# Optimization experiments

Hardware: AMD Instinct MI355X
Metric: run time of the kernel (lower is better)

The kernel has to match this reference:

```python
import jax, jax.numpy as jnp
import numpy as np

B, C, H, W = 4, 64, 128, 128
D_INNER, D_STATE, DT_RANK, K = 192, 16, 6, 4  # d_model = 3*C//2 = 96, expand = 2
EPS = 1e-5


def _haar():
    # pywt db1: dec_lo=[s,s], dec_hi=[-s,s]; code reverses dec_* and uses rec_* in
    # original order -> for Haar both dec and rec filter banks are identical.
    s = np.float32(1.0 / np.sqrt(2.0))
    lo = np.array([s, s], np.float32)
    hi = np.array([s, -s], np.float32)
    # stack order: [lo(i)lo(j), hi(i)lo(j), lo(i)hi(j), hi(i)hi(j)]
    return np.stack([np.outer(lo, lo), np.outer(hi, lo),
                     np.outer(lo, hi), np.outer(hi, hi)], 0)  # (4,2,2)

DEC = jnp.asarray(_haar())
REC = jnp.asarray(_haar())
DN = ('NCHW', 'OIHW', 'NCHW')


def _ln(x, s, b):
    m = x.mean(-1, keepdims=True)
    v = x.var(-1, keepdims=True)
    return (x - m) * jax.lax.rsqrt(v + EPS) * s + b


def _wt(x):
    b, c, h, w = x.shape
    wf = jnp.tile(DEC[:, None], (c, 1, 1, 1))  # (4c,1,2,2), groups=c, pad=0 for db1
    y = jax.lax.conv_general_dilated(x, wf, (2, 2), 'VALID',
                                     feature_group_count=c, dimension_numbers=DN)
    return y.reshape(b, c, 4, h // 2, w // 2)


def _iwt(x):
    # conv_transpose2d(stride=2, pad=0, groups=c) == lhs-dilated conv with flipped kernel, pad k-1
    b, c = x.shape[0], x.shape[1]
    h2, w2 = x.shape[3], x.shape[4]
    xr = x.reshape(b, c * 4, h2, w2)
    wf = jnp.tile(REC[:, ::-1, ::-1][None], (c, 1, 1, 1))  # (c,4,2,2)
    return jax.lax.conv_general_dilated(xr, wf, (1, 1), ((1, 1), (1, 1)),
                                        lhs_dilation=(2, 2), feature_group_count=c,
                                        dimension_numbers=DN)


def _ss2d(x, in_proj_w, conv_dw_w, conv_dw_b, x_proj_w, dt_proj_w, dt_proj_b,
          A_log, Ds, out_norm_s, out_norm_b, out_proj_w):
    b, d, h, w = x.shape  # d == D_INNER
    L = h * w
    xz = jnp.einsum('bchw,ec->behw', x, in_proj_w)  # (b,2d,h,w)
    x1, z = xz[:, :d], xz[:, d:]
    x1 = jax.lax.conv_general_dilated(x1, conv_dw_w, (1, 1), ((1, 1), (1, 1)),
                                      feature_group_count=d, dimension_numbers=DN)
    x1 = jax.nn.silu(x1 + conv_dw_b[None, :, None, None])
    # 4-direction flattening: hw, wh, and their reverses
    xf = x1.reshape(b, d, L)
    xt = x1.transpose(0, 1, 3, 2).reshape(b, d, L)
    xs = jnp.stack([xf, xt], 1)
    xs = jnp.concatenate([xs, xs[..., ::-1]], 1)  # (b,K,d,L)
    x_dbl = jnp.einsum('bkdl,kcd->bkcl', xs, x_proj_w)
    dts = x_dbl[:, :, :DT_RANK]
    Bs = x_dbl[:, :, DT_RANK:DT_RANK + D_STATE]   # (b,K,n,L)
    Cs = x_dbl[:, :, DT_RANK + D_STATE:]
    delta = jax.nn.softplus(jnp.einsum('bkrl,kdr->bkdl', dts, dt_proj_w)
                            + dt_proj_b[None, :, :, None])
    A = -jnp.exp(A_log)  # (K,d,n)

    def step(hc, inp):
        d_t, u_t, b_t, c_t = inp  # (b,K,d),(b,K,d),(b,K,n),(b,K,n)
        dA = jnp.exp(d_t[..., None] * A[None])
        hc = hc * dA + (d_t * u_t)[..., None] * b_t[:, :, None, :]
        y = jnp.einsum('bkdn,bkn->bkd', hc, c_t)
        return hc, y

    h0 = jnp.zeros((b, K, d, D_STATE), x.dtype)
    inputs = (delta.transpose(3, 0, 1, 2), xs.transpose(3, 0, 1, 2),
              Bs.transpose(3, 0, 1, 2), Cs.transpose(3, 0, 1, 2))
    _, ys = jax.lax.scan(step, h0, inputs)            # (L,b,K,d)
    out_y = ys.transpose(1, 2, 3, 0) + xs * Ds[None, :, :, None]  # (b,K,d,L)
    inv_y = out_y[:, 2:][..., ::-1]
    wh = out_y[:, 1].reshape(b, d, w, h).transpose(0, 1, 3, 2).reshape(b, d, L)
    invwh = inv_y[:, 1].reshape(b, d, w, h).transpose(0, 1, 3, 2).reshape(b, d, L)
    y = out_y[:, 0] + inv_y[:, 0] + wh + invwh        # (b,d,L)
    y = _ln(y.reshape(b, d, h, w).transpose(0, 2, 3, 1), out_norm_s, out_norm_b)
    y = y * jax.nn.silu(z.transpose(0, 2, 3, 1))
    y = jnp.einsum('bhwd,ed->bhwe', y, out_proj_w)
    return y.transpose(0, 3, 1, 2)


def reference(x, wt_low_scale, wt_high_scale, low_conv_w, in_proj_w, conv_dw_w,
              conv_dw_b, x_proj_w, dt_proj_w, dt_proj_b, A_log, Ds,
              out_norm_s, out_norm_b, out_proj_w, ln2_s, ln2_b, eca_w):
    b, c = x.shape[0], x.shape[1]
    wt = _wt(x)                                       # (b,c,4,h2,w2)
    h2, w2 = wt.shape[3], wt.shape[4]
    low = wt[:, :, 0] * wt_low_scale
    high = wt[:, :, 1:].reshape(b, c * 3, h2, w2) * wt_high_scale
    low = jax.nn.silu(jnp.einsum('bchw,ec->behw', low, low_conv_w[:, :, 0, 0]))
    high = _ss2d(high, in_proj_w, conv_dw_w, conv_dw_b, x_proj_w, dt_proj_w,
                 dt_proj_b, A_log, Ds, out_norm_s, out_norm_b, out_proj_w)
    high = _ln(high.transpose(0, 2, 3, 1), ln2_s, ln2_b).transpose(0, 3, 1, 2)
    mamba = jnp.tile(low, (1, 3, 1, 1)) * high
    merged = jnp.concatenate([low, mamba], 1).reshape(b, c, 4, h2, w2)
    y = _iwt(merged)                                  # (b,c,h,w)
    # ECA: gap -> conv1d(k=5) over channels -> sigmoid gate
    pooled = y.mean((2, 3))[:, None, :]               # (b,1,c)
    att = jax.lax.conv_general_dilated(pooled, eca_w.reshape(1, 1, 5), (1,),
                                       ((2, 2),), dimension_numbers=('NCH', 'OIH', 'NCH'))
    att = jax.nn.sigmoid(att[:, 0])
    return y * att[:, :, None, None] + x


def setup_inputs():
    key = jax.random.key(0)
    ks = jax.random.split(key, 20)
    f = jax.random.normal
    return {
        'x': f(ks[0], (B, C, H, W), jnp.float32),
        'wt_low_scale': jax.random.uniform(ks[1], (1, C, 1, 1), jnp.float32),
        'wt_high_scale': jax.random.uniform(ks[2], (1, 3 * C, 1, 1), jnp.float32),
        'low_conv_w': f(ks[3], (C, C, 1, 1), jnp.float32) * 0.1,
        'in_proj_w': f(ks[4], (2 * D_INNER, D_INNER), jnp.float32) * 0.05,
        'conv_dw_w': f(ks[5], (D_INNER, 1, 3, 3), jnp.float32) * 0.3,
        'conv_dw_b': f(ks[6], (D_INNER,), jnp.float32) * 0.1,
        'x_proj_w': f(ks[7], (K, DT_RANK + 2 * D_STATE, D_INNER), jnp.float32) * 0.05,
        'dt_proj_w': f(ks[8], (K, D_INNER, DT_RANK), jnp.float32) * 0.1,
        'dt_proj_b': jax.random.uniform(ks[9], (K, D_INNER), jnp.float32) - 4.0,
        'A_log': jax.random.uniform(ks[10], (K, D_INNER, D_STATE), jnp.float32),
        'Ds': f(ks[11], (K, D_INNER), jnp.float32) * 0.1,
        'out_norm_s': jnp.ones((D_INNER,), jnp.float32),
        'out_norm_b': jnp.zeros((D_INNER,), jnp.float32),
        'out_proj_w': f(ks[12], (D_INNER, D_INNER), jnp.float32) * 0.05,
        'ln2_s': jnp.ones((3 * C,), jnp.float32),
        'ln2_b': jnp.zeros((3 * C,), jnp.float32),
        'eca_w': f(ks[13], (5,), jnp.float32) * 0.3,
    }
```

## Files before the change

kernel.cpp:

```cpp
#include <hip/hip_runtime.h>

constexpr int cB = 4, cC = 64, cH = 128, cW = 128;
constexpr int cL = 4096;
constexpr int cD = 192, cN = 16;
constexpr int NCH = 64, CHUNK = 64;

__device__ __forceinline__ float silu_f(float v) { return v / (1.f + __expf(-v)); }

__global__ __launch_bounds__(256) void k_wt(const float* __restrict__ x,
                                            const float* __restrict__ wls,
                                            const float* __restrict__ whs,
                                            float* __restrict__ lraw,
                                            float* __restrict__ high) {
    int idx = blockIdx.x * 256 + threadIdx.x;
    int j = idx & 63, i = (idx >> 6) & 63, c = (idx >> 12) & 63, b = idx >> 18;
    const float* xp = x + (((size_t)(b * cC + c)) * cH + 2 * i) * cW + 2 * j;
    float x00 = xp[0], x01 = xp[1], x10 = xp[cW], x11 = xp[cW + 1];
    float s0 = 0.5f * (x00 + x01 + x10 + x11);
    float s1 = 0.5f * (x00 + x01 - x10 - x11);
    float s2 = 0.5f * (x00 - x01 + x10 - x11);
    float s3 = 0.5f * (x00 - x01 - x10 + x11);
    int l = i * 64 + j;
    lraw[(size_t)(b * cC + c) * cL + l] = s0 * wls[c];
    int ch = c * 3;
    high[(size_t)(b * cD + ch + 0) * cL + l] = s1 * whs[ch + 0];
    high[(size_t)(b * cD + ch + 1) * cL + l] = s2 * whs[ch + 1];
    high[(size_t)(b * cD + ch + 2) * cL + l] = s3 * whs[ch + 2];
}

__global__ __launch_bounds__(256) void k_lowconv(const float* __restrict__ lraw,
                                                 const float* __restrict__ w,
                                                 float* __restrict__ lowT) {
    int bid = blockIdx.x;
    int lt0 = (bid & 63) * 64;
    int b = bid >> 6;
    __shared__ float sW[16][68];
    __shared__ float sI[16][65];
    int tid = threadIdx.x, lt = tid & 63, eg = tid >> 6;
    float acc[16];
#pragma unroll
    for (int m = 0; m < 16; m++) acc[m] = 0.f;
    for (int c0 = 0; c0 < 64; c0 += 16) {
#pragma unroll
        for (int q = 0; q < 4; q++) {
            int tt = tid + q * 256;
            int cc = tt & 15, ee = tt >> 4;
            sW[cc][ee] = w[ee * 64 + c0 + cc];
        }
#pragma unroll
        for (int q = 0; q < 4; q++) {
            int tt = tid + q * 256;
            int ll = tt & 63, cc = tt >> 6;
            sI[cc][ll] = lraw[(size_t)(b * cC + c0 + cc) * cL + lt0 + ll];
        }
        __syncthreads();
#pragma unroll
        for (int cc = 0; cc < 16; cc++) {
            float iv = sI[cc][lt];
#pragma unroll
            for (int m = 0; m < 16; m++) acc[m] = fmaf(sW[cc][eg * 16 + m], iv, acc[m]);
        }
        __syncthreads();
    }
#pragma unroll
    for (int m = 0; m < 16; m++) {
        int e = eg * 16 + m;
        lowT[((size_t)b * cL + lt0 + lt) * 64 + e] = silu_f(acc[m]);
    }
}

__global__ __launch_bounds__(256) void k_inproj(const float* __restrict__ hi,
                                                const float* __restrict__ w,
                                                float* __restrict__ xout,
                                                float* __restrict__ zT) {
    int bid = blockIdx.x;
    int lt0 = (bid & 63) * 64;
    int et = (bid >> 6) % 6;
    int b = bid / (6 * 64);
    int e0 = et * 64;
    __shared__ float sW[16][68];
    __shared__ float sI[16][65];
    int tid = threadIdx.x, lt = tid & 63, eg = tid >> 6;
    float acc[16];
#pragma unroll
    for (int m = 0; m < 16; m++) acc[m] = 0.f;
    for (int c0 = 0; c0 < 192; c0 += 16) {
#pragma unroll
        for (int q = 0; q < 4; q++) {
            int tt = tid + q * 256;
            int cc = tt & 15, ee = tt >> 4;
            sW[cc][ee] = w[(e0 + ee) * 192 + c0 + cc];
        }
#pragma unroll
        for (int q = 0; q < 4; q++) {
            int tt = tid + q * 256;
            int ll = tt & 63, cc = tt >> 6;
            sI[cc][ll] = hi[(size_t)(b * cD + c0 + cc) * cL + lt0 + ll];
        }
        __syncthreads();
#pragma unroll
        for (int cc = 0; cc < 16; cc++) {
            float iv = sI[cc][lt];
#pragma unroll
            for (int m = 0; m < 16; m++) acc[m] = fmaf(sW[cc][eg * 16 + m], iv, acc[m]);
        }
        __syncthreads();
    }
#pragma unroll
    for (int m = 0; m < 16; m++) {
        int e = e0 + eg * 16 + m;
        float v = acc[m];
        if (e < 192) xout[(size_t)(b * cD + e) * cL + lt0 + lt] = v;
        else zT[((size_t)b * cL + lt0 + lt) * 192 + (e - 192)] = v;
    }
}

__global__ __launch_bounds__(256) void k_dwconv(const float* __restrict__ xin,
                                                const float* __restrict__ w,
                                                const float* __restrict__ bias,
                                                float* __restrict__ x1,
                                                float* __restrict__ u1) {
    int bd = blockIdx.x;
    int d = bd % cD;
    const float* xp = xin + (size_t)bd * cL;
    float wv[9];
#pragma unroll
    for (int t = 0; t < 9; t++) wv[t] = w[d * 9 + t];
    float bv = bias[d];
    __shared__ float sm[64][65];
    int tid = threadIdx.x;
#pragma unroll
    for (int q = 0; q < 16; q++) {
        int p = tid + q * 256;
        int i = p >> 6, j = p & 63;
        float acc = bv;
#pragma unroll
        for (int di = 0; di < 3; di++) {
            int ii = i + di - 1;
            if (ii < 0 || ii >= 64) continue;
#pragma unroll
            for (int dj = 0; dj < 3; dj++) {
                int jj = j + dj - 1;
                if (jj < 0 || jj >= 64) continue;
                acc = fmaf(wv[di * 3 + dj], xp[ii * 64 + jj], acc);
            }
        }
        sm[i][j] = silu_f(acc);
    }
    __syncthreads();
#pragma unroll
    for (int q = 0; q < 16; q++) {
        int p = tid + q * 256;
        x1[(size_t)bd * cL + p] = sm[p >> 6][p & 63];
        u1[(size_t)bd * cL + p] = sm[p & 63][p >> 6];
    }
}

__global__ __launch_bounds__(256) void k_xproj(const float* __restrict__ x1,
                                               const float* __restrict__ u1,
                                               const float* __restrict__ xpw,
                                               float* __restrict__ xdbl) {
    int bid = blockIdx.x;
    int lt0 = (bid & 63) * 64;
    int k = (bid >> 6) & 3;
    int b = bid >> 8;
    const float* src = (k & 1) ? u1 : x1;
    bool rev = (k >= 2);
    __shared__ float sW[16][68];
    __shared__ float sI[16][65];
    int tid = threadIdx.x, lt = tid & 63, eg = tid >> 6;
    float acc[16];
#pragma unroll
    for (int m = 0; m < 16; m++) acc[m] = 0.f;
    for (int c0 = 0; c0 < 192; c0 += 16) {
#pragma unroll
        for (int q = 0; q < 4; q++) {
            int tt = tid + q * 256;
            int cc = tt & 15, ee = tt >> 4;
            sW[cc][ee] = (ee < 38) ? xpw[(k * 38 + ee) * 192 + c0 + cc] : 0.f;
        }
#pragma unroll
        for (int q = 0; q < 4; q++) {
            int tt = tid + q * 256;
            int ll = tt & 63, cc = tt >> 6;
            int l = lt0 + ll;
            int lm = rev ? (cL - 1 - l) : l;
            sI[cc][ll] = src[(size_t)(b * cD + c0 + cc) * cL + lm];
        }
        __syncthreads();
#pragma unroll
        for (int cc = 0; cc < 16; cc++) {
            float iv = sI[cc][lt];
#pragma unroll
            for (int m = 0; m < 16; m++) acc[m] = fmaf(sW[cc][eg * 16 + m], iv, acc[m]);
        }
        __syncthreads();
    }
#pragma unroll
    for (int m = 0; m < 16; m++) {
        int e = eg * 16 + m;
        if (e < 38) xdbl[(size_t)((b * 4 + k) * 38 + e) * cL + lt0 + lt] = acc[m];
    }
}

__global__ __launch_bounds__(384) void k_scan1(const float* __restrict__ xdbl,
                                               const float* __restrict__ x1,
                                               const float* __restrict__ u1,
                                               const float* __restrict__ dtw,
                                               const float* __restrict__ dtb,
                                               const float* __restrict__ alog,
                                               float* __restrict__ P,
                                               float* __restrict__ S) {
    int bid = blockIdx.x;
    int ch = bid % NCH;
    int bk = bid / NCH;
    int k = bk & 3, b = bk >> 2;
    int tid = threadIdx.x;
    int d = tid % 192, nh = tid / 192;
    int n0 = nh * 8;
    float Av2[8], h[8], Pe[8];
#pragma unroll
    for (int j = 0; j < 8; j++) {
        Av2[j] = -__expf(alog[(k * 192 + d) * 16 + n0 + j]) * 1.44269504088896f;
        h[j] = 0.f;
        Pe[j] = 0.f;
    }
    float dtbv = dtb[k * 192 + d];
    float dtwv[6];
#pragma unroll
    for (int r = 0; r < 6; r++) dtwv[r] = dtw[(k * 192 + d) * 6 + r];
    const float* dtrows = xdbl + (size_t)(bk * 38) * cL;
    const float* Brow = xdbl + (size_t)(bk * 38 + 6) * cL;
    const float* usrc = ((k & 1) ? u1 : x1) + (size_t)b * cD * cL;
    bool rev = (k >= 2);

    __shared__ float su[192][17];
    __shared__ float sB[16][16];
    __shared__ float sdt[16][8];

    int p0 = ch * CHUNK;
    for (int t0 = p0; t0 < p0 + CHUNK; t0 += 16) {
#pragma unroll
        for (int pp = 0; pp < 8; pp++) {
            int row = pp * 24 + (tid >> 4);
            int col = tid & 15;
            su[row][col] = usrc[(size_t)row * cL + (rev ? (cL - 1 - (t0 + col)) : (t0 + col))];
        }
        if (tid < 256) sB[tid & 15][tid >> 4] = Brow[(size_t)(tid >> 4) * cL + t0 + (tid & 15)];
        if (tid < 96) sdt[tid & 15][tid >> 4] = dtrows[(size_t)(tid >> 4) * cL + t0 + (tid & 15)];
        __syncthreads();
#pragma unroll
        for (int l = 0; l < 16; l++) {
            float uv = su[d][l];
            float acc = dtbv;
#pragma unroll
            for (int r = 0; r < 6; r++) acc = fmaf(dtwv[r], sdt[l][r], acc);
            float sp = fmaxf(acc, 0.f) + __logf(1.f + __expf(-fabsf(acc)));
            float duB = sp * uv;
            float Bv[8];
            *reinterpret_cast<float4*>(&Bv[0]) = *reinterpret_cast<const float4*>(&sB[l][n0]);
            *reinterpret_cast<float4*>(&Bv[4]) = *reinterpret_cast<const float4*>(&sB[l][n0 + 4]);
#pragma unroll
            for (int j = 0; j < 8; j++) {
                float e = sp * Av2[j];
                Pe[j] += e;
                float dA = exp2f(e);
                h[j] = fmaf(h[j], dA, duB * Bv[j]);
            }
        }
        __syncthreads();
    }
    size_t base = (size_t)bid * 16 * 192 + d;
#pragma unroll
    for (int j = 0; j < 8; j++) {
        P[base + (size_t)(n0 + j) * 192] = exp2f(Pe[j]);
        S[base + (size_t)(n0 + j) * 192] = h[j];
    }
}

__global__ __launch_bounds__(256) void k_carry(const float* __restrict__ P,
                                               float* __restrict__ S) {
    int gid = blockIdx.x * 256 + threadIdx.x;
    int d = gid % 192;
    int n = (gid / 192) & 15;
    int bk = gid / 3072;
    float h = 0.f;
    for (int c = 0; c < NCH; c++) {
        size_t idx = ((size_t)(bk * NCH + c) * 16 + n) * 192 + d;
        h = fmaf(P[idx], h, S[idx]);
        S[idx] = h;
    }
}

__global__ __launch_bounds__(384) void k_scan2(const float* __restrict__ xdbl,
                                               const float* __restrict__ x1,
                                               const float* __restrict__ u1,
                                               const float* __restrict__ dtw,
                                               const float* __restrict__ dtb,
                                               const float* __restrict__ alog,
                                               const float* __restrict__ dss,
                                               const float* __restrict__ S,
                                               float* __restrict__ yacc) {
    int bid = blockIdx.x;
    int ch = bid % NCH;
    int bk = bid / NCH;
    int k = bk & 3, b = bk >> 2;
    int tid = threadIdx.x;
    int d = tid % 192, nh = tid / 192;
    int n0 = nh * 8;
    float Av2[8], h[8];
#pragma unroll
    for (int j = 0; j < 8; j++) {
        Av2[j] = -__expf(alog[(k * 192 + d) * 16 + n0 + j]) * 1.44269504088896f;
        h[j] = (ch == 0) ? 0.f : S[((size_t)(bk * NCH + ch - 1) * 16 + n0 + j) * 192 + d];
    }
    float Dv = dss[k * 192 + d];
    float dtbv = dtb[k * 192 + d];
    float dtwv[6];
#pragma unroll
    for (int r = 0; r < 6; r++) dtwv[r] = dtw[(k * 192 + d) * 6 + r];
    const float* dtrows = xdbl + (size_t)(bk * 38) * cL;
    const float* Brow = xdbl + (size_t)(bk * 38 + 6) * cL;
    const float* Crow = xdbl + (size_t)(bk * 38 + 22) * cL;
    const float* usrc = ((k & 1) ? u1 : x1) + (size_t)b * cD * cL;
    bool rev = (k >= 2);

    __shared__ float su[192][17];
    __shared__ float sB[16][16];
    __shared__ float sC[16][16];
    __shared__ float sdt[16][8];

    int p0 = ch * CHUNK;
    for (int t0 = p0; t0 < p0 + CHUNK; t0 += 16) {
#pragma unroll
        for (int pp = 0; pp < 8; pp++) {
            int row = pp * 24 + (tid >> 4);
            int col = tid & 15;
            su[row][col] = usrc[(size_t)row * cL + (rev ? (cL - 1 - (t0 + col)) : (t0 + col))];
        }
        if (tid < 256) {
            sB[tid & 15][tid >> 4] = Brow[(size_t)(tid >> 4) * cL + t0 + (tid & 15)];
            sC[tid & 15][tid >> 4] = Crow[(size_t)(tid >> 4) * cL + t0 + (tid & 15)];
        }
        if (tid < 96) sdt[tid & 15][tid >> 4] = dtrows[(size_t)(tid >> 4) * cL + t0 + (tid & 15)];
        __syncthreads();
#pragma unroll
        for (int l = 0; l < 16; l++) {
            float uv = su[d][l];
            float acc = dtbv;
#pragma unroll
            for (int r = 0; r < 6; r++) acc = fmaf(dtwv[r], sdt[l][r], acc);
            float sp = fmaxf(acc, 0.f) + __logf(1.f + __expf(-fabsf(acc)));
            float duB = sp * uv;
            float Bv[8], Cv[8];
            *reinterpret_cast<float4*>(&Bv[0]) = *reinterpret_cast<const float4*>(&sB[l][n0]);
            *reinterpret_cast<float4*>(&Bv[4]) = *reinterpret_cast<const float4*>(&sB[l][n0 + 4]);
            *reinterpret_cast<float4*>(&Cv[0]) = *reinterpret_cast<const float4*>(&sC[l][n0]);
            *reinterpret_cast<float4*>(&Cv[4]) = *reinterpret_cast<const float4*>(&sC[l][n0 + 4]);
            float y = (nh == 0) ? uv * Dv : 0.f;
#pragma unroll
            for (int j = 0; j < 8; j++) {
                float dA = exp2f(sp * Av2[j]);
                h[j] = fmaf(h[j], dA, duB * Bv[j]);
                y = fmaf(h[j], Cv[j], y);
            }
            int lg = t0 + l;
            int lm;
            if (k == 0) lm = lg;
            else if (k == 1) lm = (lg & 63) * 64 + (lg >> 6);
            else if (k == 2) lm = cL - 1 - lg;
            else { int q = cL - 1 - lg; lm = (q & 63) * 64 + (q >> 6); }
            atomicAdd(&yacc[((size_t)b * cL + lm) * 192 + d], y);
        }
        __syncthreads();
    }
}

__global__ __launch_bounds__(256) void k_comb(const float* __restrict__ yacc,
                                              const float* __restrict__ zT,
                                              const float* __restrict__ ons,
                                              const float* __restrict__ onb,
                                              float* __restrict__ yln) {
    int bid = blockIdx.x;
    int b = bid >> 10;
    int pg = bid & 1023;
    int tid = threadIdx.x;
    int wq = tid >> 6, lane = tid & 63;
    int l = pg * 4 + wq;
    float v[3];
    float s = 0.f, s2 = 0.f;
#pragma unroll
    for (int m = 0; m < 3; m++) {
        int d = lane + 64 * m;
        float t = yacc[((size_t)b * cL + l) * 192 + d];
        v[m] = t;
        s += t;
        s2 += t * t;
    }
#pragma unroll
    for (int o = 1; o < 64; o <<= 1) {
        s += __shfl_xor(s, o);
        s2 += __shfl_xor(s2, o);
    }
    float mean = s / 192.f;
    float var = s2 / 192.f - mean * mean;
    float rstd = rsqrtf(var + 1e-5f);
#pragma unroll
    for (int m = 0; m < 3; m++) {
        int d = lane + 64 * m;
        float zv = zT[((size_t)b * cL + l) * 192 + d];
        float yn = (v[m] - mean) * rstd * ons[d] + onb[d];
        yln[((size_t)b * cL + l) * 192 + d] = yn * silu_f(zv);
    }
}

__global__ __launch_bounds__(256) void k_outproj(const float* __restrict__ yln,
                                                 const float* __restrict__ w,
                                                 float* __restrict__ hout) {
    int bid = blockIdx.x;
    int lt0 = (bid & 63) * 64;
    int et = (bid >> 6) % 3;
    int b = bid / 192;
    int e0 = et * 64;
    __shared__ float sW[16][68];
    __shared__ float sI[16][65];
    int tid = threadIdx.x, lt = tid & 63, eg = tid >> 6;
    float acc[16];
#pragma unroll
    for (int m = 0; m < 16; m++) acc[m] = 0.f;
    for (int c0 = 0; c0 < 192; c0 += 16) {
#pragma unroll
        for (int q = 0; q < 4; q++) {
            int tt = tid + q * 256;
            int cc = tt & 15, ee = tt >> 4;
            sW[cc][ee] = w[(e0 + ee) * 192 + c0 + cc];
        }
#pragma unroll
        for (int q = 0; q < 4; q++) {
            int tt = tid + q * 256;
            int cc = tt & 15, lq = tt >> 4;
            sI[cc][lq] = yln[((size_t)b * cL + lt0 + lq) * 192 + c0 + cc];
        }
        __syncthreads();
#pragma unroll
        for (int cc = 0; cc < 16; cc++) {
            float iv = sI[cc][lt];
#pragma unroll
            for (int m = 0; m < 16; m++) acc[m] = fmaf(sW[cc][eg * 16 + m], iv, acc[m]);
        }
        __syncthreads();
    }
#pragma unroll
    for (int m = 0; m < 16; m++) {
        hout[((size_t)b * cL + lt0 + lt) * 192 + e0 + eg * 16 + m] = acc[m];
    }
}

__global__ __launch_bounds__(256) void k_ln2(const float* __restrict__ hout,
                                             const float* __restrict__ lowT,
                                             const float* __restrict__ l2s,
                                             const float* __restrict__ l2b,
                                             float* __restrict__ merged) {
    int bid = blockIdx.x;
    int b = bid >> 10;
    int pg = bid & 1023;
    int tid = threadIdx.x;
    int wq = tid >> 6, lane = tid & 63;
    int l = pg * 4 + wq;
    float v[3];
    float s = 0.f, s2 = 0.f;
#pragma unroll
    for (int m = 0; m < 3; m++) {
        int d = lane + 64 * m;
        float t = hout[((size_t)b * cL + l) * 192 + d];
        v[m] = t;
        s += t;
        s2 += t * t;
    }
#pragma unroll
    for (int o = 1; o < 64; o <<= 1) {
        s += __shfl_xor(s, o);
        s2 += __shfl_xor(s2, o);
    }
    float mean = s / 192.f;
    float var = s2 / 192.f - mean * mean;
    float rstd = rsqrtf(var + 1e-5f);
    float lv = lowT[((size_t)b * cL + l) * 64 + lane];
    float* mp = merged + ((size_t)b * cL + l) * 256;
    mp[lane] = lv;
#pragma unroll
    for (int m = 0; m < 3; m++) {
        int d = lane + 64 * m;
        float hn = (v[m] - mean) * rstd * l2s[d] + l2b[d];
        mp[64 + d] = lv * hn;
    }
}

__global__ __launch_bounds__(256) void k_iwt(const float* __restrict__ merged,
                                             float* __restrict__ ypre) {
    int idx = blockIdx.x * 256 + threadIdx.x;
    int j = idx & 63, i = (idx >> 6) & 63, g = (idx >> 12) & 63, b = idx >> 18;
    const float4 mv = *reinterpret_cast<const float4*>(merged + ((size_t)b * cL + i * 64 + j) * 256 + g * 4);
    float m0 = mv.x, m1 = mv.y, m2 = mv.z, m3 = mv.w;
    float* yp = ypre + ((size_t)(b * 64 + g) * cH + 2 * i) * cW + 2 * j;
    float2 r0 = make_float2(0.5f * (m0 + m1 + m2 + m3), 0.5f * (m0 + m1 - m2 - m3));
    float2 r1 = make_float2(0.5f * (m0 - m1 + m2 - m3), 0.5f * (m0 - m1 - m2 + m3));
    *reinterpret_cast<float2*>(yp) = r0;
    *reinterpret_cast<float2*>(yp + cW) = r1;
}

__global__ __launch_bounds__(256) void k_pool(const float* __restrict__ ypre,
                                              float* __restrict__ pooled) {
    int bg = blockIdx.x;
    const float* p = ypre + (size_t)bg * (cH * cW);
    float s = 0.f;
    for (int t = threadIdx.x; t < cH * cW; t += 256) s += p[t];
#pragma unroll
    for (int o = 1; o < 64; o <<= 1) s += __shfl_xor(s, o);
    __shared__ float red[4];
    if ((threadIdx.x & 63) == 0) red[threadIdx.x >> 6] = s;
    __syncthreads();
    if (threadIdx.x == 0) pooled[bg] = (red[0] + red[1] + red[2] + red[3]) * (1.f / (cH * cW));
}

__global__ __launch_bounds__(256) void k_eca(const float* __restrict__ pooled,
                                             const float* __restrict__ w,
                                             float* __restrict__ att) {
    int t = threadIdx.x;
    int b = t >> 6, c = t & 63;
    float s = 0.f;
#pragma unroll
    for (int u = 0; u < 5; u++) {
        int cc = c + u - 2;
        if (cc >= 0 && cc < 64) s += w[u] * pooled[b * 64 + cc];
    }
    att[t] = 1.f / (1.f + __expf(-s));
}

__global__ __launch_bounds__(256) void k_final(const float* __restrict__ ypre,
                                               const float* __restrict__ x,
                                               const float* __restrict__ att,
                                               float* __restrict__ out) {
    int idx = blockIdx.x * 256 + threadIdx.x;
    size_t base = (size_t)idx * 4;
    int bc = (int)(base >> 14);
    float a = att[bc];
    float4 yv = *reinterpret_cast<const float4*>(ypre + base);
    float4 xv = *reinterpret_cast<const float4*>(x + base);
    float4 o;
    o.x = fmaf(yv.x, a, xv.x);
    o.y = fmaf(yv.y, a, xv.y);
    o.z = fmaf(yv.z, a, xv.z);
    o.w = fmaf(yv.w, a, xv.w);
    *reinterpret_cast<float4*>(out + base) = o;
}

extern "C" void kernel_launch(void* const* d_in, const int* in_sizes, int n_in,
                              void* d_out, int out_size, void* d_ws, size_t ws_size,
                              hipStream_t stream) {
    const float* x    = (const float*)d_in[0];
    const float* wls  = (const float*)d_in[1];
    const float* whs  = (const float*)d_in[2];
    const float* lcw  = (const float*)d_in[3];
    const float* ipw  = (const float*)d_in[4];
    const float* dww  = (const float*)d_in[5];
    const float* dwb  = (const float*)d_in[6];
    const float* xpw  = (const float*)d_in[7];
    const float* dtw  = (const float*)d_in[8];
    const float* dtb  = (const float*)d_in[9];
    const float* alog = (const float*)d_in[10];
    const float* dss  = (const float*)d_in[11];
    const float* ons  = (const float*)d_in[12];
    const float* onb  = (const float*)d_in[13];
    const float* opw  = (const float*)d_in[14];
    const float* l2s  = (const float*)d_in[15];
    const float* l2b  = (const float*)d_in[16];
    const float* ecw  = (const float*)d_in[17];
    float* out = (float*)d_out;
    float* w = (float*)d_ws;

    float* high   = w + 0;
    float* lraw   = w + 3145728;
    float* lowT   = w + 4194304;
    float* xbuf   = w + 5242880;
    float* zT     = w + 8388608;
    float* x1     = w + 11534336;
    float* u1     = w + 14680064;
    float* yacc   = w + 17825792;
    float* Sbuf   = w + 20971520;
    float* xdbl   = high;
    float* Pbuf   = xbuf;
    float* yln    = xbuf;
    float* hout   = high;
    float* merged = x1;
    float* ypre   = yacc;
    float* pooled = lraw;
    float* att    = lraw + 256;

    k_wt<<<4096, 256, 0, stream>>>(x, wls, whs, lraw, high);
    k_lowconv<<<256, 256, 0, stream>>>(lraw, lcw, lowT);
    k_inproj<<<1536, 256, 0, stream>>>(high, ipw, xbuf, zT);
    k_dwconv<<<768, 256, 0, stream>>>(xbuf, dww, dwb, x1, u1);
    k_xproj<<<1024, 256, 0, stream>>>(x1, u1, xpw, xdbl);
    hipMemsetAsync(yacc, 0, (size_t)cB * cL * cD * sizeof(float), stream);
    k_scan1<<<1024, 384, 0, stream>>>(xdbl, x1, u1, dtw, dtb, alog, Pbuf, Sbuf);
    k_carry<<<192, 256, 0, stream>>>(Pbuf, Sbuf);
    k_scan2<<<1024, 384, 0, stream>>>(xdbl, x1, u1, dtw, dtb, alog, dss, Sbuf, yacc);
    k_comb<<<4096, 256, 0, stream>>>(yacc, zT, ons, onb, yln);
    k_outproj<<<768, 256, 0, stream>>>(yln, opw, hout);
    k_ln2<<<4096, 256, 0, stream>>>(hout, lowT, l2s, l2b, merged);
    k_iwt<<<4096, 256, 0, stream>>>(merged, ypre);
    k_pool<<<256, 256, 0, stream>>>(ypre, pooled);
    k_eca<<<1, 256, 0, stream>>>(pooled, ecw, att);
    k_final<<<4096, 256, 0, stream>>>(ypre, x, att, out);
}
```

Baseline: 455.3 us.

## Double-buffer scan chunk loads through registers and batch softplus in scan kernels

Both chunked selective-scan kernels now prefetch the next 16-step tile of u, B, C and dt into registers while the current tile is processed from a double-buffered shared-memory copy. This removes the second barrier per tile and hides global-load latency behind the recurrence. The softplus of dt is computed for eight steps at once to expose more independent work before the serial state update. The in-projection kernel also reorders its block index so the six output-channel tiles of one position tile run adjacently, which may improve input reuse in cache. The cost is twice the shared memory and more registers, which may lower occupancy.

Result: no change. 452.6 us (-0.6%).

```diff
diff --git a/kernel.cpp b/kernel.cpp
--- a/kernel.cpp
+++ b/kernel.cpp
@@ -74,9 +74,10 @@
                                                 float* __restrict__ xout,
                                                 float* __restrict__ zT) {
     int bid = blockIdx.x;
-    int lt0 = (bid & 63) * 64;
-    int et = (bid >> 6) % 6;
-    int b = bid / (6 * 64);
+    int et = bid % 6;
+    int blt = bid / 6;
+    int lt0 = (blt & 63) * 64;
+    int b = blt >> 6;
     int e0 = et * 64;
     __shared__ float sW[16][68];
     __shared__ float sI[16][65];
@@ -234,41 +235,69 @@
     const float* usrc = ((k & 1) ? u1 : x1) + (size_t)b * cD * cL;
     bool rev = (k >= 2);
 
-    __shared__ float su[192][17];
-    __shared__ float sB[16][16];
-    __shared__ float sdt[16][8];
-
+    __shared__ float su[2][192][17];
+    __shared__ float sB[2][16][16];
+    __shared__ float sdt[2][16][8];
+
+    int rowA = tid >> 4, colA = tid & 15;
     int p0 = ch * CHUNK;
+    float r_su[8], r_b, r_dt;
+
+    {
+        int t0 = p0;
+#pragma unroll
+        for (int pp = 0; pp < 8; pp++) {
+            int row = pp * 24 + rowA;
+            r_su[pp] = usrc[(size_t)row * cL + (rev ? (cL - 1 - (t0 + colA)) : (t0 + colA))];
+        }
+        if (tid < 256) r_b = Brow[(size_t)rowA * cL + t0 + colA];
+        if (tid < 96)  r_dt = dtrows[(size_t)rowA * cL + t0 + colA];
+    }
+    int cur = 0;
     for (int t0 = p0; t0 < p0 + CHUNK; t0 += 16) {
 #pragma unroll
-        for (int pp = 0; pp < 8; pp++) {
-            int row = pp * 24 + (tid >> 4);
-            int col = tid & 15;
-            su[row][col] = usrc[(size_t)row * cL + (rev ? (cL - 1 - (t0 + col)) : (t0 + col))];
-        }
-        if (tid < 256) sB[tid & 15][tid >> 4] = Brow[(size_t)(tid >> 4) * cL + t0 + (tid & 15)];
-        if (tid < 96) sdt[tid & 15][tid >> 4] = dtrows[(size_t)(tid >> 4) * cL + t0 + (tid & 15)];
-        __syncthreads();
-#pragma unroll
-        for (int l = 0; l < 16; l++) {
-            float uv = su[d][l];
-            float acc = dtbv;
-#pragma unroll
-            for (int r = 0; r < 6; r++) acc = fmaf(dtwv[r], sdt[l][r], acc);
-            float sp = fmaxf(acc, 0.f) + __logf(1.f + __expf(-fabsf(acc)));
-            float duB = sp * uv;
-            float Bv[8];
-            *reinterpret_cast<float4*>(&Bv[0]) = *reinterpret_cast<const float4*>(&sB[l][n0]);
-            *reinterpret_cast<float4*>(&Bv[4]) = *reinterpret_cast<const float4*>(&sB[l][n0 + 4]);
-#pragma unroll
-            for (int j = 0; j < 8; j++) {
-                float e = sp * Av2[j];
-                Pe[j] += e;
-                float dA = exp2f(e);
-                h[j] = fmaf(h[j], dA, duB * Bv[j]);
-            }
-        }
-        __syncthreads();
+        for (int pp = 0; pp < 8; pp++) su[cur][pp * 24 + rowA][colA] = r_su[pp];
+        if (tid < 256) sB[cur][colA][rowA] = r_b;
+        if (tid < 96)  sdt[cur][colA][rowA] = r_dt;
+        __syncthreads();
+        if (t0 + 16 < p0 + CHUNK) {
+            int t1 = t0 + 16;
+#pragma unroll
+            for (int pp = 0; pp < 8; pp++) {
+                int row = pp * 24 + rowA;
+                r_su[pp] = usrc[(size_t)row * cL + (rev ? (cL - 1 - (t1 + colA)) : (t1 + colA))];
+            }
+            if (tid < 256) r_b = Brow[(size_t)rowA * cL + t1 + colA];
+            if (tid < 96)  r_dt = dtrows[(size_t)rowA * cL + t1 + colA];
+        }
+#pragma unroll
+        for (int hh = 0; hh < 2; hh++) {
+            float sp[8];
+#pragma unroll
+            for (int q = 0; q < 8; q++) {
+                int l = hh * 8 + q;
+                float acc = dtbv;
+#pragma unroll
+                for (int r = 0; r < 6; r++) acc = fmaf(dtwv[r], sdt[cur][l][r], acc);
+                sp[q] = fmaxf(acc, 0.f) + __logf(1.f + __expf(-fabsf(acc)));
+            }
+#pragma unroll
+            for (int q = 0; q < 8; q++) {
+                int l = hh * 8 + q;
+                float uv = su[cur][d][l];
+                float duB = sp[q] * uv;
+                float Bv[8];
+                *reinterpret_cast<float4*>(&Bv[0]) = *reinterpret_cast<const float4*>(&sB[cur][l][n0]);
+                *reinterpret_cast<float4*>(&Bv[4]) = *reinterpret_cast<const float4*>(&sB[cur][l][n0 + 4]);
+#pragma unroll
+                for (int j = 0; j < 8; j++) {
+                    float e = sp[q] * Av2[j];
+                    Pe[j] += e;
+                    h[j] = fmaf(h[j], exp2f(e), duB * Bv[j]);
+                }
+            }
+        }
+        cur ^= 1;
     }
     size_t base = (size_t)bid * 16 * 192 + d;
 #pragma unroll
@@ -325,54 +354,88 @@
     const float* usrc = ((k & 1) ? u1 : x1) + (size_t)b * cD * cL;
     bool rev = (k >= 2);
 
-    __shared__ float su[192][17];
-    __shared__ float sB[16][16];
-    __shared__ float sC[16][16];
-    __shared__ float sdt[16][8];
-
+    __shared__ float su[2][192][17];
+    __shared__ float sB[2][16][16];
+    __shared__ float sC[2][16][16];
+    __shared__ float sdt[2][16][8];
+
+    int rowA = tid >> 4, colA = tid & 15;
     int p0 = ch * CHUNK;
+    float r_su[8], r_b, r_c, r_dt;
+
+    {
+        int t0 = p0;
+#pragma unroll
+        for (int pp = 0; pp < 8; pp++) {
+            int row = pp * 24 + rowA;
+            r_su[pp] = usrc[(size_t)row * cL + (rev ? (cL - 1 - (t0 + colA)) : (t0 + colA))];
+        }
+        if (tid < 256) {
+            r_b = Brow[(size_t)rowA * cL + t0 + colA];
+            r_c = Crow[(size_t)rowA * cL + t0 + colA];
+        }
+        if (tid < 96) r_dt = dtrows[(size_t)rowA * cL + t0 + colA];
+    }
+    int cur = 0;
     for (int t0 = p0; t0 < p0 + CHUNK; t0 += 16) {
 #pragma unroll
-        for (int pp = 0; pp < 8; pp++) {
-            int row = pp * 24 + (tid >> 4);
-            int col = tid & 15;
-            su[row][col] = usrc[(size_t)row * cL + (rev ? (cL - 1 - (t0 + col)) : (t0 + col))];
-        }
+        for (int pp = 0; pp < 8; pp++) su[cur][pp * 24 + rowA][colA] = r_su[pp];
         if (tid < 256) {
-            sB[tid & 15][tid >> 4] = Brow[(size_t)(tid >> 4) * cL + t0 + (tid & 15)];
-            sC[tid & 15][tid >> 4] = Crow[(size_t)(tid >> 4) * cL + t0 + (tid & 15)];
-        }
-        if (tid < 96) sdt[tid & 15][tid >> 4] = dtrows[(size_t)(tid >> 4) * cL + t0 + (tid & 15)];
-        __syncthreads();
-#pragma unroll
-        for (int l = 0; l < 16; l++) {
-            float uv = su[d][l];
-            float acc = dtbv;
-#pragma unroll
-            for (int r = 0; r < 6; r++) acc = fmaf(dtwv[r], sdt[l][r], acc);
-            float sp = fmaxf(acc, 0.f) + __logf(1.f + __expf(-fabsf(acc)));
-            float duB = sp * uv;
-            float Bv[8], Cv[8];
-            *reinterpret_cast<float4*>(&Bv[0]) = *reinterpret_cast<const float4*>(&sB[l][n0]);
-            *reinterpret_cast<float4*>(&Bv[4]) = *reinterpret_cast<const float4*>(&sB[l][n0 + 4]);
-            *reinterpret_cast<float4*>(&Cv[0]) = *reinterpret_cast<const float4*>(&sC[l][n0]);
-            *reinterpret_cast<float4*>(&Cv[4]) = *reinterpret_cast<const float4*>(&sC[l][n0 + 4]);
-            float y = (nh == 0) ? uv * Dv : 0.f;
-#pragma unroll
-            for (int j = 0; j < 8; j++) {
-                float dA = exp2f(sp * Av2[j]);
-                h[j] = fmaf(h[j], dA, duB * Bv[j]);
-                y = fmaf(h[j], Cv[j], y);
-            }
-            int lg = t0 + l;
-            int lm;
-            if (k == 0) lm = lg;
-            else if (k == 1) lm = (lg & 63) * 64 + (lg >> 6);
-            else if (k == 2) lm = cL - 1 - lg;
-            else { int q = cL - 1 - lg; lm = (q & 63) * 64 + (q >> 6); }
-            atomicAdd(&yacc[((size_t)b * cL + lm) * 192 + d], y);
-        }
-        __syncthreads();
+            sB[cur][colA][rowA] = r_b;
+            sC[cur][colA][rowA] = r_c;
+        }
+        if (tid < 96) sdt[cur][colA][rowA] = r_dt;
+        __syncthreads();
+        if (t0 + 16 < p0 + CHUNK) {
+            int t1 = t0 + 16;
+#pragma unroll
+            for (int pp = 0; pp < 8; pp++) {
+                int row = pp * 24 + rowA;
+                r_su[pp] = usrc[(size_t)row * cL + (rev ? (cL - 1 - (t1 + colA)) : (t1 + colA))];
+            }
+            if (tid < 256) {
+                r_b = Brow[(size_t)rowA * cL + t1 + colA];
+                r_c = Crow[(size_t)rowA * cL + t1 + colA];
+            }
+            if (tid < 96) r_dt = dtrows[(size_t)rowA * cL + t1 + colA];
+        }
+#pragma unroll
+        for (int hh = 0; hh < 2; hh++) {
+            float sp[8];
+#pragma unroll
+            for (int q = 0; q < 8; q++) {
+                int l = hh * 8 + q;
+                float acc = dtbv;
+#pragma unroll
+                for (int r = 0; r < 6; r++) acc = fmaf(dtwv[r], sdt[cur][l][r], acc);
+                sp[q] = fmaxf(acc, 0.f) + __logf(1.f + __expf(-fabsf(acc)));
+            }
+#pragma unroll
+            for (int q = 0; q < 8; q++) {
+                int l = hh * 8 + q;
+                float uv = su[cur][d][l];
+                float duB = sp[q] * uv;
+                float Bv[8], Cv[8];
+                *reinterpret_cast<float4*>(&Bv[0]) = *reinterpret_cast<const float4*>(&sB[cur][l][n0]);
+                *reinterpret_cast<float4*>(&Bv[4]) = *reinterpret_cast<const float4*>(&sB[cur][l][n0 + 4]);
+                *reinterpret_cast<float4*>(&Cv[0]) = *reinterpret_cast<const float4*>(&sC[cur][l][n0]);
+                *reinterpret_cast<float4*>(&Cv[4]) = *reinterpret_cast<const float4*>(&sC[cur][l][n0 + 4]);
+                float y = (nh == 0) ? uv * Dv : 0.f;
+#pragma unroll
+                for (int j = 0; j < 8; j++) {
+                    h[j] = fmaf(h[j], exp2f(sp[q] * Av2[j]), duB * Bv[j]);
+                    y = fmaf(h[j], Cv[j], y);
+                }
+                int lg = t0 + hh * 8 + q;
+                int lm;
+                if (k == 0) lm = lg;
+                else if (k == 1) lm = (lg & 63) * 64 + (lg >> 6);
+                else if (k == 2) lm = cL - 1 - lg;
+                else { int qq = cL - 1 - lg; lm = (qq & 63) * 64 + (qq >> 6); }
+                atomicAdd(&yacc[((size_t)b * cL + lm) * 192 + d], y);
+            }
+        }
+        cur ^= 1;
     }
 }
 
```

## Restructure chunked selective scan into zero-init scan plus carry-correction pass

Applied to the files above, without the earlier changes.

The two-pass chunked scan (state pass, carry, output pass with carried state) becomes a zero-initial-state scan that emits outputs and chunk-end states directly. A light correction kernel then adds the carried-in state contribution C·exp(A·cumsum(dt))·h_prev. The correction needs no u or B loads and no full recurrence, so the second pass does far less work. The carry kernel rebuilds chunk decay from a per-d dt sum rather than a stored per-(n,d) product. Chunks are halved to get more blocks, the atomicAdd traffic is halved by first combining the two n-halves in shared memory, and the in_proj block order is remapped. The cost is a second round of atomics into yacc.

New measurement: 523.0 us. 1.15x slower.

```diff
diff --git a/kernel.cpp b/kernel.cpp
--- a/kernel.cpp
+++ b/kernel.cpp
@@ -3,7 +3,7 @@
 constexpr int cB = 4, cC = 64, cH = 128, cW = 128;
 constexpr int cL = 4096;
 constexpr int cD = 192, cN = 16;
-constexpr int NCH = 64, CHUNK = 64;
+constexpr int NCH = 128, CHUNK = 32;
 
 __device__ __forceinline__ float silu_f(float v) { return v / (1.f + __expf(-v)); }
 
@@ -74,9 +74,10 @@
                                                 float* __restrict__ xout,
                                                 float* __restrict__ zT) {
     int bid = blockIdx.x;
-    int lt0 = (bid & 63) * 64;
-    int et = (bid >> 6) % 6;
-    int b = bid / (6 * 64);
+    int et = bid % 6;
+    int blt = bid / 6;
+    int lt0 = (blt & 63) * 64;
+    int b = blt >> 6;
     int e0 = et * 64;
     __shared__ float sW[16][68];
     __shared__ float sI[16][65];
@@ -203,103 +204,15 @@
     }
 }
 
-__global__ __launch_bounds__(384) void k_scan1(const float* __restrict__ xdbl,
-                                               const float* __restrict__ x1,
-                                               const float* __restrict__ u1,
-                                               const float* __restrict__ dtw,
-                                               const float* __restrict__ dtb,
-                                               const float* __restrict__ alog,
-                                               float* __restrict__ P,
-                                               float* __restrict__ S) {
-    int bid = blockIdx.x;
-    int ch = bid % NCH;
-    int bk = bid / NCH;
-    int k = bk & 3, b = bk >> 2;
-    int tid = threadIdx.x;
-    int d = tid % 192, nh = tid / 192;
-    int n0 = nh * 8;
-    float Av2[8], h[8], Pe[8];
-#pragma unroll
-    for (int j = 0; j < 8; j++) {
-        Av2[j] = -__expf(alog[(k * 192 + d) * 16 + n0 + j]) * 1.44269504088896f;
-        h[j] = 0.f;
-        Pe[j] = 0.f;
-    }
-    float dtbv = dtb[k * 192 + d];
-    float dtwv[6];
-#pragma unroll
-    for (int r = 0; r < 6; r++) dtwv[r] = dtw[(k * 192 + d) * 6 + r];
-    const float* dtrows = xdbl + (size_t)(bk * 38) * cL;
-    const float* Brow = xdbl + (size_t)(bk * 38 + 6) * cL;
-    const float* usrc = ((k & 1) ? u1 : x1) + (size_t)b * cD * cL;
-    bool rev = (k >= 2);
-
-    __shared__ float su[192][17];
-    __shared__ float sB[16][16];
-    __shared__ float sdt[16][8];
-
-    int p0 = ch * CHUNK;
-    for (int t0 = p0; t0 < p0 + CHUNK; t0 += 16) {
-#pragma unroll
-        for (int pp = 0; pp < 8; pp++) {
-            int row = pp * 24 + (tid >> 4);
-            int col = tid & 15;
-            su[row][col] = usrc[(size_t)row * cL + (rev ? (cL - 1 - (t0 + col)) : (t0 + col))];
-        }
-        if (tid < 256) sB[tid & 15][tid >> 4] = Brow[(size_t)(tid >> 4) * cL + t0 + (tid & 15)];
-        if (tid < 96) sdt[tid & 15][tid >> 4] = dtrows[(size_t)(tid >> 4) * cL + t0 + (tid & 15)];
-        __syncthreads();
-#pragma unroll
-        for (int l = 0; l < 16; l++) {
-            float uv = su[d][l];
-            float acc = dtbv;
-#pragma unroll
-            for (int r = 0; r < 6; r++) acc = fmaf(dtwv[r], sdt[l][r], acc);
-            float sp = fmaxf(acc, 0.f) + __logf(1.f + __expf(-fabsf(acc)));
-            float duB = sp * uv;
-            float Bv[8];
-            *reinterpret_cast<float4*>(&Bv[0]) = *reinterpret_cast<const float4*>(&sB[l][n0]);
-            *reinterpret_cast<float4*>(&Bv[4]) = *reinterpret_cast<const float4*>(&sB[l][n0 + 4]);
-#pragma unroll
-            for (int j = 0; j < 8; j++) {
-                float e = sp * Av2[j];
-                Pe[j] += e;
-                float dA = exp2f(e);
-                h[j] = fmaf(h[j], dA, duB * Bv[j]);
-            }
-        }
-        __syncthreads();
-    }
-    size_t base = (size_t)bid * 16 * 192 + d;
-#pragma unroll
-    for (int j = 0; j < 8; j++) {
-        P[base + (size_t)(n0 + j) * 192] = exp2f(Pe[j]);
-        S[base + (size_t)(n0 + j) * 192] = h[j];
-    }
-}
-
-__global__ __launch_bounds__(256) void k_carry(const float* __restrict__ P,
-                                               float* __restrict__ S) {
-    int gid = blockIdx.x * 256 + threadIdx.x;
-    int d = gid % 192;
-    int n = (gid / 192) & 15;
-    int bk = gid / 3072;
-    float h = 0.f;
-    for (int c = 0; c < NCH; c++) {
-        size_t idx = ((size_t)(bk * NCH + c) * 16 + n) * 192 + d;
-        h = fmaf(P[idx], h, S[idx]);
-        S[idx] = h;
-    }
-}
-
-__global__ __launch_bounds__(384) void k_scan2(const float* __restrict__ xdbl,
+__global__ __launch_bounds__(384) void k_scanA(const float* __restrict__ xdbl,
                                                const float* __restrict__ x1,
                                                const float* __restrict__ u1,
                                                const float* __restrict__ dtw,
                                                const float* __restrict__ dtb,
                                                const float* __restrict__ alog,
                                                const float* __restrict__ dss,
-                                               const float* __restrict__ S,
+                                               float* __restrict__ S,
+                                               float* __restrict__ Qb,
                                                float* __restrict__ yacc) {
     int bid = blockIdx.x;
     int ch = bid % NCH;
@@ -312,7 +225,7 @@
 #pragma unroll
     for (int j = 0; j < 8; j++) {
         Av2[j] = -__expf(alog[(k * 192 + d) * 16 + n0 + j]) * 1.44269504088896f;
-        h[j] = (ch == 0) ? 0.f : S[((size_t)(bk * NCH + ch - 1) * 16 + n0 + j) * 192 + d];
+        h[j] = 0.f;
     }
     float Dv = dss[k * 192 + d];
     float dtbv = dtb[k * 192 + d];
@@ -329,48 +242,168 @@
     __shared__ float sB[16][16];
     __shared__ float sC[16][16];
     __shared__ float sdt[16][8];
-
+    __shared__ float sy[192][17];
+
+    int rowA = tid >> 4, colA = tid & 15;
     int p0 = ch * CHUNK;
+    float Q = 0.f;
     for (int t0 = p0; t0 < p0 + CHUNK; t0 += 16) {
 #pragma unroll
         for (int pp = 0; pp < 8; pp++) {
-            int row = pp * 24 + (tid >> 4);
-            int col = tid & 15;
-            su[row][col] = usrc[(size_t)row * cL + (rev ? (cL - 1 - (t0 + col)) : (t0 + col))];
+            int row = pp * 24 + rowA;
+            su[row][colA] = usrc[(size_t)row * cL + (rev ? (cL - 1 - (t0 + colA)) : (t0 + colA))];
         }
         if (tid < 256) {
-            sB[tid & 15][tid >> 4] = Brow[(size_t)(tid >> 4) * cL + t0 + (tid & 15)];
-            sC[tid & 15][tid >> 4] = Crow[(size_t)(tid >> 4) * cL + t0 + (tid & 15)];
-        }
-        if (tid < 96) sdt[tid & 15][tid >> 4] = dtrows[(size_t)(tid >> 4) * cL + t0 + (tid & 15)];
-        __syncthreads();
+            sB[colA][rowA] = Brow[(size_t)rowA * cL + t0 + colA];
+            sC[colA][rowA] = Crow[(size_t)rowA * cL + t0 + colA];
+        }
+        if (tid < 96) sdt[colA][rowA] = dtrows[(size_t)rowA * cL + t0 + colA];
+        __syncthreads();
+        float yv[16];
 #pragma unroll
         for (int l = 0; l < 16; l++) {
-            float uv = su[d][l];
             float acc = dtbv;
 #pragma unroll
             for (int r = 0; r < 6; r++) acc = fmaf(dtwv[r], sdt[l][r], acc);
             float sp = fmaxf(acc, 0.f) + __logf(1.f + __expf(-fabsf(acc)));
+            Q += sp;
+            float uv = su[d][l];
             float duB = sp * uv;
             float Bv[8], Cv[8];
             *reinterpret_cast<float4*>(&Bv[0]) = *reinterpret_cast<const float4*>(&sB[l][n0]);
             *reinterpret_cast<float4*>(&Bv[4]) = *reinterpret_cast<const float4*>(&sB[l][n0 + 4]);
             *reinterpret_cast<float4*>(&Cv[0]) = *reinterpret_cast<const float4*>(&sC[l][n0]);
             *reinterpret_cast<float4*>(&Cv[4]) = *reinterpret_cast<const float4*>(&sC[l][n0 + 4]);
-            float y = (nh == 0) ? uv * Dv : 0.f;
-#pragma unroll
-            for (int j = 0; j < 8; j++) {
-                float dA = exp2f(sp * Av2[j]);
-                h[j] = fmaf(h[j], dA, duB * Bv[j]);
-                y = fmaf(h[j], Cv[j], y);
+            float yA = 0.f, yB = 0.f;
+#pragma unroll
+            for (int j = 0; j < 4; j++) {
+                h[j] = fmaf(h[j], exp2f(sp * Av2[j]), duB * Bv[j]);
+                yA = fmaf(h[j], Cv[j], yA);
             }
-            int lg = t0 + l;
-            int lm;
-            if (k == 0) lm = lg;
-            else if (k == 1) lm = (lg & 63) * 64 + (lg >> 6);
-            else if (k == 2) lm = cL - 1 - lg;
-            else { int q = cL - 1 - lg; lm = (q & 63) * 64 + (q >> 6); }
-            atomicAdd(&yacc[((size_t)b * cL + lm) * 192 + d], y);
+#pragma unroll
+            for (int j = 4; j < 8; j++) {
+                h[j] = fmaf(h[j], exp2f(sp * Av2[j]), duB * Bv[j]);
+                yB = fmaf(h[j], Cv[j], yB);
+            }
+            yv[l] = yA + yB + ((nh == 0) ? uv * Dv : 0.f);
+        }
+        if (nh == 1) {
+#pragma unroll
+            for (int l = 0; l < 16; l++) sy[d][l] = yv[l];
+        }
+        __syncthreads();
+        if (nh == 0) {
+#pragma unroll
+            for (int l = 0; l < 16; l++) {
+                int lg = t0 + l;
+                int lm;
+                if (k == 0) lm = lg;
+                else if (k == 1) lm = (lg & 63) * 64 + (lg >> 6);
+                else if (k == 2) lm = cL - 1 - lg;
+                else { int qq = cL - 1 - lg; lm = (qq & 63) * 64 + (qq >> 6); }
+                atomicAdd(&yacc[((size_t)b * cL + lm) * 192 + d], yv[l] + sy[d][l]);
+            }
+        }
+        __syncthreads();
+    }
+    size_t base = (size_t)bid * 16 * 192 + d;
+#pragma unroll
+    for (int j = 0; j < 8; j++) S[base + (size_t)(n0 + j) * 192] = h[j];
+    if (nh == 0) Qb[(size_t)bid * 192 + d] = Q;
+}
+
+__global__ __launch_bounds__(256) void k_carryQ(const float* __restrict__ alog,
+                                                const float* __restrict__ Qb,
+                                                float* __restrict__ S) {
+    int gid = blockIdx.x * 256 + threadIdx.x;
+    int d = gid % 192;
+    int n = (gid / 192) & 15;
+    int bk = gid / 3072;
+    int k = bk & 3;
+    float Av2 = -__expf(alog[(k * 192 + d) * 16 + n]) * 1.44269504088896f;
+    float h = 0.f;
+    for (int c = 0; c < NCH; c++) {
+        size_t qidx = (size_t)(bk * NCH + c) * 192 + d;
+        size_t idx = ((size_t)(bk * NCH + c) * 16 + n) * 192 + d;
+        h = fmaf(exp2f(Av2 * Qb[qidx]), h, S[idx]);
+        S[idx] = h;
+    }
+}
+
+__global__ __launch_bounds__(384) void k_scanC(const float* __restrict__ xdbl,
+                                               const float* __restrict__ dtw,
+                                               const float* __restrict__ dtb,
+                                               const float* __restrict__ alog,
+                                               const float* __restrict__ S,
+                                               float* __restrict__ yacc) {
+    int bid = blockIdx.x;
+    int ch = bid % NCH;
+    int bk = bid / NCH;
+    int k = bk & 3, b = bk >> 2;
+    int tid = threadIdx.x;
+    int d = tid % 192, nh = tid / 192;
+    int n0 = nh * 8;
+
+    __shared__ float sC[16][16];
+    __shared__ float sdt[16][8];
+    __shared__ float sy[192][17];
+
+    if (ch == 0) return;
+
+    float Av2[8], hc[8];
+#pragma unroll
+    for (int j = 0; j < 8; j++) {
+        Av2[j] = -__expf(alog[(k * 192 + d) * 16 + n0 + j]) * 1.44269504088896f;
+        hc[j] = S[((size_t)(bk * NCH + ch - 1) * 16 + n0 + j) * 192 + d];
+    }
+    float dtbv = dtb[k * 192 + d];
+    float dtwv[6];
+#pragma unroll
+    for (int r = 0; r < 6; r++) dtwv[r] = dtw[(k * 192 + d) * 6 + r];
+    const float* dtrows = xdbl + (size_t)(bk * 38) * cL;
+    const float* Crow = xdbl + (size_t)(bk * 38 + 22) * cL;
+
+    int rowA = tid >> 4, colA = tid & 15;
+    int p0 = ch * CHUNK;
+    float Q = 0.f;
+    for (int t0 = p0; t0 < p0 + CHUNK; t0 += 16) {
+        if (tid < 256) sC[colA][rowA] = Crow[(size_t)rowA * cL + t0 + colA];
+        if (tid < 96) sdt[colA][rowA] = dtrows[(size_t)rowA * cL + t0 + colA];
+        __syncthreads();
+        float cv[16];
+#pragma unroll
+        for (int l = 0; l < 16; l++) {
+            float acc = dtbv;
+#pragma unroll
+            for (int r = 0; r < 6; r++) acc = fmaf(dtwv[r], sdt[l][r], acc);
+            float sp = fmaxf(acc, 0.f) + __logf(1.f + __expf(-fabsf(acc)));
+            Q += sp;
+            float Cv[8];
+            *reinterpret_cast<float4*>(&Cv[0]) = *reinterpret_cast<const float4*>(&sC[l][n0]);
+            *reinterpret_cast<float4*>(&Cv[4]) = *reinterpret_cast<const float4*>(&sC[l][n0 + 4]);
+            float cA = 0.f, cB = 0.f;
+#pragma unroll
+            for (int j = 0; j < 4; j++) cA = fmaf(exp2f(Q * Av2[j]), hc[j] * Cv[j], cA);
+#pragma unroll
+            for (int j = 4; j < 8; j++) cB = fmaf(exp2f(Q * Av2[j]), hc[j] * Cv[j], cB);
+            cv[l] = cA + cB;
+        }
+        if (nh == 1) {
+#pragma unroll
+            for (int l = 0; l < 16; l++) sy[d][l] = cv[l];
+        }
+        __syncthreads();
+        if (nh == 0) {
+#pragma unroll
+            for (int l = 0; l < 16; l++) {
+                int lg = t0 + l;
+                int lm;
+                if (k == 0) lm = lg;
+                else if (k == 1) lm = (lg & 63) * 64 + (lg >> 6);
+                else if (k == 2) lm = cL - 1 - lg;
+                else { int qq = cL - 1 - lg; lm = (qq & 63) * 64 + (qq >> 6); }
+                atomicAdd(&yacc[((size_t)b * cL + lm) * 192 + d], cv[l] + sy[d][l]);
+            }
         }
         __syncthreads();
     }
@@ -588,8 +621,8 @@
     float* u1     = w + 14680064;
     float* yacc   = w + 17825792;
     float* Sbuf   = w + 20971520;
+    float* Qbuf   = w + 27262976;
     float* xdbl   = high;
-    float* Pbuf   = xbuf;
     float* yln    = xbuf;
     float* hout   = high;
     float* merged = x1;
@@ -603,9 +636,9 @@
     k_dwconv<<<768, 256, 0, stream>>>(xbuf, dww, dwb, x1, u1);
     k_xproj<<<1024, 256, 0, stream>>>(x1, u1, xpw, xdbl);
     hipMemsetAsync(yacc, 0, (size_t)cB * cL * cD * sizeof(float), stream);
-    k_scan1<<<1024, 384, 0, stream>>>(xdbl, x1, u1, dtw, dtb, alog, Pbuf, Sbuf);
-    k_carry<<<192, 256, 0, stream>>>(Pbuf, Sbuf);
-    k_scan2<<<1024, 384, 0, stream>>>(xdbl, x1, u1, dtw, dtb, alog, dss, Sbuf, yacc);
+    k_scanA<<<2048, 384, 0, stream>>>(xdbl, x1, u1, dtw, dtb, alog, dss, Sbuf, Qbuf, yacc);
+    k_carryQ<<<192, 256, 0, stream>>>(alog, Qbuf, Sbuf);
+    k_scanC<<<2048, 384, 0, stream>>>(xdbl, dtw, dtb, alog, Sbuf, yacc);
     k_comb<<<4096, 256, 0, stream>>>(yacc, zT, ons, onb, yln);
     k_outproj<<<768, 256, 0, stream>>>(yln, opw, hout);
     k_ln2<<<4096, 256, 0, stream>>>(hout, lowT, l2s, l2b, merged);
```
